# Performance work log

Measured on AMD Instinct MI355X. Metric: run time of the kernel, lower is better.

Reference implementation:

```python
import jax, jax.numpy as jnp
import numpy as np

N_NODES = 100_000
N_EDGES = 1_600_000
NUM_GRAPHS = 512
D1, D2, D3, D5, NUM_CLASSES = 3, 50, 15, 10, 6
BN_EPS = 1e-5


def setup_inputs() -> dict:
    key = jax.random.key(0)
    ks = jax.random.split(key, 16)

    def w(k, shape):
        fan_in = shape[0]
        return jax.random.normal(k, shape, jnp.float32) / np.sqrt(fan_in).astype(np.float32)

    return {
        "x": jax.random.normal(ks[0], (N_NODES, D1), jnp.float32),
        "edge_attr": jax.random.normal(ks[1], (N_EDGES, D1), jnp.float32),
        # edge MLP: Lin(9,50) -> ReLU -> Lin(50,15)
        "edge_w1": w(ks[2], (3 * D1, D2)), "edge_b1": jnp.zeros((D2,), jnp.float32),
        "edge_w2": w(ks[3], (D2, D3)), "edge_b2": jnp.zeros((D3,), jnp.float32),
        # node MLP: Lin(18,50) -> ReLU -> Lin(50,15)
        "node_w1": w(ks[4], (D1 + D3, D2)), "node_b1": jnp.zeros((D2,), jnp.float32),
        "node_w2": w(ks[5], (D2, D3)), "node_b2": jnp.zeros((D3,), jnp.float32),
        # readout head
        "fc1_w": w(ks[6], (D3, D5)), "fc1_b": jnp.zeros((D5,), jnp.float32),
        "bn_gamma": jnp.ones((D5,), jnp.float32), "bn_beta": jnp.zeros((D5,), jnp.float32),
        "fc2_w": w(ks[7], (D5, NUM_CLASSES)), "fc2_b": jnp.zeros((NUM_CLASSES,), jnp.float32),
        # graph structure
        "edge_index": jax.random.randint(ks[8], (2, N_EDGES), 0, N_NODES, jnp.int32),
        "batch": jnp.sort(jax.random.randint(ks[9], (N_NODES,), 0, NUM_GRAPHS, jnp.int32)),
    }


def _segment_mean(vals, idx, num_segments):
    s = jax.ops.segment_sum(vals, idx, num_segments=num_segments)
    c = jax.ops.segment_sum(jnp.ones((vals.shape[0], 1), vals.dtype), idx,
                            num_segments=num_segments)
    return s / jnp.maximum(c, 1.0)


def reference(x, edge_attr,
              edge_w1, edge_b1, edge_w2, edge_b2,
              node_w1, node_b1, node_w2, node_b2,
              fc1_w, fc1_b, bn_gamma, bn_beta, fc2_w, fc2_b,
              edge_index, batch):
    row, col = edge_index[0], edge_index[1]
    # edge model: cat([x[row], x[col], edge_attr]) -> MLP  -> [E, D3]
    e_in = jnp.concatenate([x[row], x[col], edge_attr], axis=1)
    edge_attr2 = jax.nn.relu(e_in @ edge_w1 + edge_b1) @ edge_w2 + edge_b2
    # node model: cat([x[col], edge_attr2]) -> MLP -> scatter_mean over row
    n_in = jnp.concatenate([x[col], edge_attr2], axis=1)  # [E, D1+D3]
    msg = jax.nn.relu(n_in @ node_w1 + node_b1) @ node_w2 + node_b2  # [E, D3]
    x2 = _segment_mean(msg, row, x.shape[0])  # [N, D3]
    # global mean pool per graph -> [G, D3]
    u = _segment_mean(x2, batch, NUM_GRAPHS)
    # head: fc1 -> BatchNorm1d (batch stats) -> relu -> fc2 -> log_softmax
    h = u @ fc1_w + fc1_b
    mu = h.mean(axis=0)
    var = h.var(axis=0)  # biased, matches BN training normalization
    h = bn_gamma * (h - mu) * jax.lax.rsqrt(var + BN_EPS) + bn_beta
    h = jax.nn.relu(h)
    logits = h @ fc2_w + fc2_b
    return jax.nn.log_softmax(logits, axis=1)
```

## Files before the change

kernel.cpp:

```cpp
#include <hip/hip_runtime.h>
#include <hip/hip_bf16.h>
#include <math.h>

#define N_NODES    100000
#define N_EDGES    1600000
#define NUM_GRAPHS 512
#define D2 50
#define D3 15
#define D5 10
#define NCLS 6
#define BN_EPS 1e-5f

#define W_EW1T 0
#define W_EW2T 2560
#define W_NW1T 3712
#define W_NW2T 6272
#define W_TOTAL 7680

#define EDGE_BLOCKS 1024
#define EDGE_WAVES  (EDGE_BLOCKS * 4)
#define TILES32     (N_EDGES / 32)

#define GPAD 17

typedef __attribute__((ext_vector_type(8))) short short8;
typedef __attribute__((ext_vector_type(4))) float float4_;
union BU { unsigned u[4]; short8 s; };

__device__ __forceinline__ unsigned short f2bf(float f) {
    __hip_bfloat16 h = __float2bfloat16(f);
    union { __hip_bfloat16 h; unsigned short u; } c; c.h = h; return c.u;
}
__device__ __forceinline__ unsigned pkbf(float a, float b) {
    unsigned r;
    asm("v_cvt_pk_bf16_f32 %0, %1, %2" : "=v"(r) : "v"(a), "v"(b));
    return r;
}
__device__ __forceinline__ unsigned bp(int s4, unsigned v) {
    return (unsigned)__builtin_amdgcn_ds_bpermute(s4, (int)v);
}

__global__ __launch_bounds__(256) void prep_kernel(
    const float* __restrict__ ew1, const float* __restrict__ eb1,
    const float* __restrict__ ew2, const float* __restrict__ eb2,
    const float* __restrict__ nw1, const float* __restrict__ nb1,
    const float* __restrict__ nw2, const float* __restrict__ nb2,
    unsigned short* __restrict__ wh,
    const float* __restrict__ x, ushort4* __restrict__ x4b,
    const int* __restrict__ edge_index, int* __restrict__ counts,
    const int* __restrict__ batch, float* __restrict__ gsum)
{
    __shared__ int bh[NUM_GRAPHS];
    int gtid = blockIdx.x * 256 + threadIdx.x;
    int gsz = gridDim.x * 256;

    for (int i = threadIdx.x; i < NUM_GRAPHS; i += 256) bh[i] = 0;
    __syncthreads();

    for (int i = gtid; i < W_TOTAL; i += gsz) {
        float v = 0.0f;
        if (i < W_EW2T) {
            int m = i / 40, k = i % 40;
            if (m < 50) {
                if (k < 3)                 v = ew1[k * 50 + m];
                else if (k == 3)           v = eb1[m];
                else if (k >= 4 && k < 7)  v = ew1[(k - 1) * 50 + m];
                else if (k >= 8 && k < 11) v = ew1[(k - 2) * 50 + m];
            }
        } else if (i < W_NW1T) {
            int j = i - W_EW2T; int m = j / 72, k = j % 72;
            if (m < 15) { if (k < 50) v = ew2[k * 15 + m]; else if (k == 50) v = eb2[m]; }
        } else if (i < W_NW2T) {
            int j = i - W_NW1T; int m = j / 40, k = j % 40;
            if (m < 50) {
                if (k < 15)                  v = nw1[(3 + k) * 50 + m];
                else if (k >= 16 && k < 19)  v = nw1[(k - 16) * 50 + m];
                else if (k == 19)            v = nb1[m];
            }
        } else if (i < 7424) {
            int j = i - W_NW2T; int m = j / 72, k = j % 72;
            if (m < 15) { if (k < 50) v = nw2[k * 15 + m]; else if (k == 50) v = nb2[m]; }
        }
        wh[i] = f2bf(v);
    }

    for (int n = gtid; n < N_NODES; n += gsz) {
        ushort4 v;
        v.x = f2bf(x[n * 3 + 0]); v.y = f2bf(x[n * 3 + 1]);
        v.z = f2bf(x[n * 3 + 2]); v.w = 0;
        x4b[n] = v;
        atomicAdd(&bh[batch[n]], 1);
    }

    for (int e = gtid; e < N_EDGES; e += gsz)
        atomicAdd(&counts[edge_index[e]], 1);

    __syncthreads();
    for (int i = threadIdx.x; i < NUM_GRAPHS; i += 256) {
        int v = bh[i];
        if (v) atomicAdd(&gsum[i * 16 + 15], (float)v);
    }
}

struct EIn { unsigned w0, w1, w2, w3, h0, h1; int g; float invd; };

__device__ __forceinline__ EIn load_in(int ebase, int n, int quad,
    const int* __restrict__ edge_index, const ushort4* __restrict__ x4b,
    const float* __restrict__ edge_attr,
    const int* __restrict__ counts, const int* __restrict__ batch)
{
    EIn r; r.w0 = r.w1 = r.w2 = r.w3 = 0; r.h0 = r.h1 = 0; r.g = 0; r.invd = 0.0f;
    int e = ebase + n;
    if (quad == 0) {
        int row = edge_index[e];
        int col = edge_index[N_EDGES + e];
        ushort4 xr = x4b[row];
        ushort4 xc = x4b[col];
        r.w0 = (unsigned)xr.x | ((unsigned)xr.y << 16);
        r.w1 = (unsigned)xr.z | (0x3F80u << 16);
        r.w2 = (unsigned)xc.x | ((unsigned)xc.y << 16);
        r.w3 = (unsigned)xc.z;
        r.g = batch[row];
        r.invd = 1.0f / (float)counts[row];
    } else if (quad == 1) {
        r.w0 = pkbf(edge_attr[e * 3 + 0], edge_attr[e * 3 + 1]);
        r.w1 = pkbf(edge_attr[e * 3 + 2], 0.0f);
    } else if (quad == 2) {
        int col = edge_index[N_EDGES + e];
        ushort4 xc = x4b[col];
        r.h0 = (unsigned)xc.x | ((unsigned)xc.y << 16);
        r.h1 = (unsigned)xc.z | (0x3F80u << 16);
    }
    return r;
}

__device__ __forceinline__ void perm64(const unsigned U[4][2], int s0, int s1, bool hi,
                                       short8& Bc0, short8& Bc1)
{
    BU b0, b1;
    {
        unsigned a0 = bp(s0, U[0][0]), a1 = bp(s0, U[1][0]);
        unsigned a2 = bp(s0, U[0][1]), a3 = bp(s0, U[1][1]);
        unsigned a4 = bp(s1, U[0][0]), a5 = bp(s1, U[1][0]);
        unsigned a6 = bp(s1, U[0][1]), a7 = bp(s1, U[1][1]);
        b0.u[0] = hi ? a1 : a0;
        b0.u[1] = hi ? a3 : a2;
        b0.u[2] = hi ? a5 : a4;
        b0.u[3] = hi ? a7 : a6;
    }
    {
        unsigned a0 = bp(s0, U[2][0]), a1 = bp(s0, U[3][0]);
        unsigned a2 = bp(s0, U[2][1]), a3 = bp(s0, U[3][1]);
        unsigned a4 = bp(s1, U[2][0]), a5 = bp(s1, U[3][0]);
        unsigned a6 = bp(s1, U[2][1]), a7 = bp(s1, U[3][1]);
        b1.u[0] = hi ? a1 : a0;
        b1.u[1] = hi ? a3 : a2;
        b1.u[2] = hi ? a5 : a4;
        b1.u[3] = hi ? a7 : a6;
    }
    Bc0 = b0.s; Bc1 = b1.s;
}

__device__ __forceinline__ short8 perm16(const unsigned U2[2], int s0, int s1,
                                         int quad, unsigned h0, unsigned h1)
{
    BU d;
    d.u[0] = bp(s0, U2[0]);
    d.u[1] = bp(s0, U2[1]);
    d.u[2] = bp(s1, U2[0]);
    d.u[3] = bp(s1, U2[1]);
    if (quad == 2) { d.u[0] = h0; d.u[1] = h1; d.u[2] = 0; d.u[3] = 0; }
    else if (quad == 3) { d.u[0] = 0; d.u[1] = 0; d.u[2] = 0; d.u[3] = 0; }
    return d.s;
}

__global__ __launch_bounds__(256) void edge_fused_kernel(
    const unsigned short* __restrict__ wh_g,
    const ushort4* __restrict__ x4b, const float* __restrict__ edge_attr,
    const int* __restrict__ edge_index,
    const int* __restrict__ counts, const int* __restrict__ batch,
    float* __restrict__ partial)
{
    __shared__ float acc[NUM_GRAPHS * GPAD];
    int tid = threadIdx.x, wave = tid >> 6, lane = tid & 63;
    int n = lane & 15, quad = lane >> 4;

    for (int i = tid; i < NUM_GRAPHS * GPAD; i += 256) acc[i] = 0.0f;
    __syncthreads();

    short8 A1[4], A3[4];
    #pragma unroll
    for (int t4 = 0; t4 < 4; t4++) {
        A1[t4] = *(const short8*)(wh_g + W_EW1T + (t4 * 16 + n) * 40 + quad * 8);
        A3[t4] = *(const short8*)(wh_g + W_NW1T + (t4 * 16 + n) * 40 + quad * 8);
    }
    short8 A2[2], A4[2];
    #pragma unroll
    for (int kc = 0; kc < 2; kc++) {
        A2[kc] = *(const short8*)(wh_g + W_EW2T + n * 72 + kc * 32 + quad * 8);
        A4[kc] = *(const short8*)(wh_g + W_NW2T + n * 72 + kc * 32 + quad * 8);
    }

    int s0 = ((quad & 1) * 32 + n) * 4;
    int s1 = s0 + 64;
    bool hi = (quad & 2) != 0;

    const float4_ Z0 = {0.f, 0.f, 0.f, 0.f};

    int t = blockIdx.x * 4 + wave;
    EIn cur0 = load_in(t * 32,      n, quad, edge_index, x4b, edge_attr, counts, batch);
    EIn cur1 = load_in(t * 32 + 16, n, quad, edge_index, x4b, edge_attr, counts, batch);

    for (;;) {
        int g0 = __shfl(cur0.g, n);
        float q0 = __shfl(cur0.invd, n);
        int g1 = __shfl(cur1.g, n);
        float q1 = __shfl(cur1.invd, n);

        int tn = t + EDGE_WAVES;
        bool more = (tn < TILES32);
        EIn nx0, nx1;
        nx0.w0 = nx0.w1 = nx0.w2 = nx0.w3 = nx0.h0 = nx0.h1 = 0; nx0.g = 0; nx0.invd = 0.f;
        nx1 = nx0;
        if (more) {
            nx0 = load_in(tn * 32,      n, quad, edge_index, x4b, edge_attr, counts, batch);
            nx1 = load_in(tn * 32 + 16, n, quad, edge_index, x4b, edge_attr, counts, batch);
        }

        BU t0, t1;
        t0.u[0] = cur0.w0; t0.u[1] = cur0.w1; t0.u[2] = cur0.w2; t0.u[3] = cur0.w3;
        t1.u[0] = cur1.w0; t1.u[1] = cur1.w1; t1.u[2] = cur1.w2; t1.u[3] = cur1.w3;
        short8 B1a = t0.s, B1b = t1.s;

        unsigned U1a[4][2], U1b[4][2];
        #pragma unroll
        for (int t4 = 0; t4 < 4; t4++) {
            float4_ za = __builtin_amdgcn_mfma_f32_16x16x32_bf16(A1[t4], B1a, Z0, 0, 0, 0);
            float4_ zb = __builtin_amdgcn_mfma_f32_16x16x32_bf16(A1[t4], B1b, Z0, 0, 0, 0);
            U1a[t4][0] = pkbf(fmaxf(za[0], 0.f), fmaxf(za[1], 0.f));
            U1a[t4][1] = pkbf(fmaxf(za[2], 0.f), fmaxf(za[3], 0.f));
            U1b[t4][0] = pkbf(fmaxf(zb[0], 0.f), fmaxf(zb[1], 0.f));
            U1b[t4][1] = pkbf(fmaxf(zb[2], 0.f), fmaxf(zb[3], 0.f));
        }

        short8 B2a0, B2a1, B2b0, B2b1;
        perm64(U1a, s0, s1, hi, B2a0, B2a1);
        perm64(U1b, s0, s1, hi, B2b0, B2b1);
        if (quad == 2) {
            BU fa, fb; fa.s = B2a1; fb.s = B2b1;
            fa.u[1] = (fa.u[1] & 0xFFFF0000u) | 0x3F80u;
            fb.u[1] = (fb.u[1] & 0xFFFF0000u) | 0x3F80u;
            B2a1 = fa.s; B2b1 = fb.s;
        }

        float4_ a2a = __builtin_amdgcn_mfma_f32_16x16x32_bf16(A2[0], B2a0, Z0, 0, 0, 0);
        float4_ a2b = __builtin_amdgcn_mfma_f32_16x16x32_bf16(A2[0], B2b0, Z0, 0, 0, 0);
        a2a = __builtin_amdgcn_mfma_f32_16x16x32_bf16(A2[1], B2a1, a2a, 0, 0, 0);
        a2b = __builtin_amdgcn_mfma_f32_16x16x32_bf16(A2[1], B2b1, a2b, 0, 0, 0);

        unsigned U2a[2] = { pkbf(a2a[0], a2a[1]), pkbf(a2a[2], a2a[3]) };
        unsigned U2b[2] = { pkbf(a2b[0], a2b[1]), pkbf(a2b[2], a2b[3]) };

        short8 B3a = perm16(U2a, s0, s1, quad, cur0.h0, cur0.h1);
        short8 B3b = perm16(U2b, s0, s1, quad, cur1.h0, cur1.h1);

        unsigned U3a[4][2], U3b[4][2];
        #pragma unroll
        for (int t4 = 0; t4 < 4; t4++) {
            float4_ za = __builtin_amdgcn_mfma_f32_16x16x32_bf16(A3[t4], B3a, Z0, 0, 0, 0);
            float4_ zb = __builtin_amdgcn_mfma_f32_16x16x32_bf16(A3[t4], B3b, Z0, 0, 0, 0);
            U3a[t4][0] = pkbf(fmaxf(za[0], 0.f), fmaxf(za[1], 0.f));
            U3a[t4][1] = pkbf(fmaxf(za[2], 0.f), fmaxf(za[3], 0.f));
            U3b[t4][0] = pkbf(fmaxf(zb[0], 0.f), fmaxf(zb[1], 0.f));
            U3b[t4][1] = pkbf(fmaxf(zb[2], 0.f), fmaxf(zb[3], 0.f));
        }

        short8 B4a0, B4a1, B4b0, B4b1;
        perm64(U3a, s0, s1, hi, B4a0, B4a1);
        perm64(U3b, s0, s1, hi, B4b0, B4b1);
        if (quad == 2) {
            BU fa, fb; fa.s = B4a1; fb.s = B4b1;
            fa.u[1] = (fa.u[1] & 0xFFFF0000u) | 0x3F80u;
            fb.u[1] = (fb.u[1] & 0xFFFF0000u) | 0x3F80u;
            B4a1 = fa.s; B4b1 = fb.s;
        }

        float4_ ma = __builtin_amdgcn_mfma_f32_16x16x32_bf16(A4[0], B4a0, Z0, 0, 0, 0);
        float4_ mb = __builtin_amdgcn_mfma_f32_16x16x32_bf16(A4[0], B4b0, Z0, 0, 0, 0);
        ma = __builtin_amdgcn_mfma_f32_16x16x32_bf16(A4[1], B4a1, ma, 0, 0, 0);
        mb = __builtin_amdgcn_mfma_f32_16x16x32_bf16(A4[1], B4b1, mb, 0, 0, 0);

        float* a0 = &acc[g0 * GPAD + quad * 4];
        float* a1 = &acc[g1 * GPAD + quad * 4];
        atomicAdd(&a0[0], ma[0] * q0);
        atomicAdd(&a0[1], ma[1] * q0);
        atomicAdd(&a0[2], ma[2] * q0);
        atomicAdd(&a1[0], mb[0] * q1);
        atomicAdd(&a1[1], mb[1] * q1);
        atomicAdd(&a1[2], mb[2] * q1);
        if (quad != 3) {
            atomicAdd(&a0[3], ma[3] * q0);
            atomicAdd(&a1[3], mb[3] * q1);
        }

        if (!more) break;
        cur0 = nx0; cur1 = nx1; t = tn;
    }

    __syncthreads();
    float* pb = partial + (size_t)blockIdx.x * (NUM_GRAPHS * 16);
    for (int i = tid; i < NUM_GRAPHS * 16; i += 256)
        pb[i] = acc[(i >> 4) * GPAD + (i & 15)];
}

__global__ __launch_bounds__(256) void reduce_kernel(
    const float* __restrict__ partial, float* __restrict__ gsum)
{
    __shared__ float red[256];
    int g = blockIdx.x;
    float s = 0.0f;
    for (int j = threadIdx.x; j < EDGE_BLOCKS * 16; j += 256) {
        int b = j >> 4, c = j & 15;
        s += partial[(size_t)b * (NUM_GRAPHS * 16) + g * 16 + c];
    }
    red[threadIdx.x] = s;
    __syncthreads();
    if (threadIdx.x < 16) {
        float t = 0.0f;
        #pragma unroll
        for (int k = 0; k < 16; k++) t += red[k * 16 + threadIdx.x];
        gsum[g * 16 + threadIdx.x] += t;
    }
}

__global__ __launch_bounds__(512) void head_kernel(
    const float* __restrict__ gsum,
    const float* __restrict__ fc1w, const float* __restrict__ fc1b,
    const float* __restrict__ gamma, const float* __restrict__ beta,
    const float* __restrict__ fc2w, const float* __restrict__ fc2b,
    float* __restrict__ out)
{
    __shared__ float ssum[D5], ssq[D5], smu[D5], sistd[D5];
    int g = threadIdx.x;
    if (g < D5) { ssum[g] = 0.0f; ssq[g] = 0.0f; }
    __syncthreads();

    const float* src = gsum + (size_t)g * 16;
    float inv = 1.0f / fmaxf(src[15], 1.0f);
    float u[D3];
    #pragma unroll
    for (int k = 0; k < D3; k++) u[k] = src[k] * inv;

    float h[D5];
    #pragma unroll
    for (int c = 0; c < D5; c++) h[c] = fc1b[c];
    #pragma unroll
    for (int k = 0; k < D3; k++) {
        float v = u[k];
        #pragma unroll
        for (int c = 0; c < D5; c++) h[c] = fmaf(v, fc1w[k * D5 + c], h[c]);
    }

    int lane = threadIdx.x & 63;
    #pragma unroll
    for (int c = 0; c < D5; c++) {
        float v = h[c];
        float v2 = v * v;
        #pragma unroll
        for (int off = 32; off >= 1; off >>= 1) {
            v  += __shfl_xor(v,  off);
            v2 += __shfl_xor(v2, off);
        }
        if (lane == 0) { atomicAdd(&ssum[c], v); atomicAdd(&ssq[c], v2); }
    }
    __syncthreads();
    if (g < D5) {
        float mu = ssum[g] * (1.0f / NUM_GRAPHS);
        float var = ssq[g] * (1.0f / NUM_GRAPHS) - mu * mu;
        smu[g] = mu;
        sistd[g] = rsqrtf(var + BN_EPS);
    }
    __syncthreads();

    float hn[D5];
    #pragma unroll
    for (int c = 0; c < D5; c++) {
        float v = gamma[c] * (h[c] - smu[c]) * sistd[c] + beta[c];
        hn[c] = fmaxf(v, 0.0f);
    }

    float lg[NCLS];
    #pragma unroll
    for (int j = 0; j < NCLS; j++) lg[j] = fc2b[j];
    #pragma unroll
    for (int c = 0; c < D5; c++) {
        float v = hn[c];
        #pragma unroll
        for (int j = 0; j < NCLS; j++) lg[j] = fmaf(v, fc2w[c * NCLS + j], lg[j]);
    }

    float m = lg[0];
    #pragma unroll
    for (int j = 1; j < NCLS; j++) m = fmaxf(m, lg[j]);
    float se = 0.0f;
    #pragma unroll
    for (int j = 0; j < NCLS; j++) se += expf(lg[j] - m);
    float lse = logf(se);
    #pragma unroll
    for (int j = 0; j < NCLS; j++) out[g * NCLS + j] = lg[j] - m - lse;
}

extern "C" void kernel_launch(void* const* d_in, const int* in_sizes, int n_in,
                              void* d_out, int out_size, void* d_ws, size_t ws_size,
                              hipStream_t stream) {
    const float* x         = (const float*)d_in[0];
    const float* edge_attr = (const float*)d_in[1];
    const float* ew1  = (const float*)d_in[2];
    const float* eb1  = (const float*)d_in[3];
    const float* ew2  = (const float*)d_in[4];
    const float* eb2  = (const float*)d_in[5];
    const float* nw1  = (const float*)d_in[6];
    const float* nb1  = (const float*)d_in[7];
    const float* nw2  = (const float*)d_in[8];
    const float* nb2  = (const float*)d_in[9];
    const float* fc1w = (const float*)d_in[10];
    const float* fc1b = (const float*)d_in[11];
    const float* gamma= (const float*)d_in[12];
    const float* beta = (const float*)d_in[13];
    const float* fc2w = (const float*)d_in[14];
    const float* fc2b = (const float*)d_in[15];
    const int* edge_index = (const int*)d_in[16];
    const int* batch      = (const int*)d_in[17];

    char* p = (char*)d_ws;
    float* partial = (float*)p;        p += (size_t)EDGE_BLOCKS * NUM_GRAPHS * 16 * sizeof(float);
    int* counts  = (int*)p;            p += (size_t)N_NODES * sizeof(int);
    ushort4* x4b = (ushort4*)p;        p += (size_t)N_NODES * sizeof(ushort4);
    float* gsum  = (float*)p;          p += (size_t)NUM_GRAPHS * 16 * sizeof(float);
    unsigned short* wh = (unsigned short*)p; p += W_TOTAL * sizeof(unsigned short);

    hipMemsetAsync(counts, 0, (size_t)N_NODES * sizeof(int), stream);
    hipMemsetAsync(gsum, 0, (size_t)NUM_GRAPHS * 16 * sizeof(float), stream);

    int egrid = (N_EDGES + 255) / 256;

    prep_kernel<<<egrid, 256, 0, stream>>>(
        ew1, eb1, ew2, eb2, nw1, nb1, nw2, nb2, wh,
        x, x4b, edge_index, counts, batch, gsum);
    edge_fused_kernel<<<EDGE_BLOCKS, 256, 0, stream>>>(
        wh, x4b, edge_attr, edge_index, counts, batch, partial);
    reduce_kernel<<<NUM_GRAPHS, 256, 0, stream>>>(partial, gsum);
    head_kernel<<<1, 512, 0, stream>>>(
        gsum, fc1w, fc1b, gamma, beta, fc2w, fc2b, (float*)d_out);
}
```

Before: 382.2 us.

## Precompute packed per-edge graph id and degree, use exact edge iteration count

Adds a pre-pass kernel that packs batch[row] and counts[row] into one 32-bit word per edge. The edge kernel then does one coalesced load instead of two dependent gathers, and swaps the divide for a hardware reciprocal. The edge grid becomes 1250 blocks so every wave gets the same number of tiles, which gives a fixed-count loop with no branch. The LDS accumulator padding also shrinks from 17 to 15. The cost is an extra kernel launch plus 6.4 MB written and read back, and the packing assumes degree below 2^23.

```diff
diff --git a/kernel.cpp b/kernel.cpp
--- a/kernel.cpp
+++ b/kernel.cpp
@@ -17,11 +17,12 @@
 #define W_NW2T 6272
 #define W_TOTAL 7680
 
-#define EDGE_BLOCKS 1024
+#define TILES32     (N_EDGES / 32)
+#define EDGE_BLOCKS 1250
 #define EDGE_WAVES  (EDGE_BLOCKS * 4)
-#define TILES32     (N_EDGES / 32)
-
-#define GPAD 17
+#define EDGE_ITERS  (TILES32 / EDGE_WAVES)
+
+#define GPAD 15
 
 typedef __attribute__((ext_vector_type(8))) short short8;
 typedef __attribute__((ext_vector_type(4))) float float4_;
@@ -102,14 +103,24 @@
     }
 }
 
-struct EIn { unsigned w0, w1, w2, w3, h0, h1; int g; float invd; };
+__global__ __launch_bounds__(256) void gd_kernel(
+    const int* __restrict__ edge_index, const int* __restrict__ counts,
+    const int* __restrict__ batch, unsigned* __restrict__ gd)
+{
+    int e = blockIdx.x * 256 + threadIdx.x;
+    if (e < N_EDGES) {
+        int row = edge_index[e];
+        gd[e] = ((unsigned)batch[row] << 23) | (unsigned)counts[row];
+    }
+}
+
+struct EIn { unsigned w0, w1, w2, w3, h0, h1, gdp; };
 
 __device__ __forceinline__ EIn load_in(int ebase, int n, int quad,
     const int* __restrict__ edge_index, const ushort4* __restrict__ x4b,
-    const float* __restrict__ edge_attr,
-    const int* __restrict__ counts, const int* __restrict__ batch)
-{
-    EIn r; r.w0 = r.w1 = r.w2 = r.w3 = 0; r.h0 = r.h1 = 0; r.g = 0; r.invd = 0.0f;
+    const float* __restrict__ edge_attr, const unsigned* __restrict__ gdb)
+{
+    EIn r; r.w0 = r.w1 = r.w2 = r.w3 = 0; r.h0 = r.h1 = 0; r.gdp = 0;
     int e = ebase + n;
     if (quad == 0) {
         int row = edge_index[e];
@@ -120,8 +131,7 @@
         r.w1 = (unsigned)xr.z | (0x3F80u << 16);
         r.w2 = (unsigned)xc.x | ((unsigned)xc.y << 16);
         r.w3 = (unsigned)xc.z;
-        r.g = batch[row];
-        r.invd = 1.0f / (float)counts[row];
+        r.gdp = gdb[e];
     } else if (quad == 1) {
         r.w0 = pkbf(edge_attr[e * 3 + 0], edge_attr[e * 3 + 1]);
         r.w1 = pkbf(edge_attr[e * 3 + 2], 0.0f);
@@ -177,8 +187,7 @@
 __global__ __launch_bounds__(256) void edge_fused_kernel(
     const unsigned short* __restrict__ wh_g,
     const ushort4* __restrict__ x4b, const float* __restrict__ edge_attr,
-    const int* __restrict__ edge_index,
-    const int* __restrict__ counts, const int* __restrict__ batch,
+    const int* __restrict__ edge_index, const unsigned* __restrict__ gdb,
     float* __restrict__ partial)
 {
     __shared__ float acc[NUM_GRAPHS * GPAD];
@@ -207,29 +216,16 @@
 
     const float4_ Z0 = {0.f, 0.f, 0.f, 0.f};
 
-    int t = blockIdx.x * 4 + wave;
-    EIn cur0 = load_in(t * 32,      n, quad, edge_index, x4b, edge_attr, counts, batch);
-    EIn cur1 = load_in(t * 32 + 16, n, quad, edge_index, x4b, edge_attr, counts, batch);
-
-    for (;;) {
-        int g0 = __shfl(cur0.g, n);
-        float q0 = __shfl(cur0.invd, n);
-        int g1 = __shfl(cur1.g, n);
-        float q1 = __shfl(cur1.invd, n);
-
-        int tn = t + EDGE_WAVES;
-        bool more = (tn < TILES32);
-        EIn nx0, nx1;
-        nx0.w0 = nx0.w1 = nx0.w2 = nx0.w3 = nx0.h0 = nx0.h1 = 0; nx0.g = 0; nx0.invd = 0.f;
-        nx1 = nx0;
-        if (more) {
-            nx0 = load_in(tn * 32,      n, quad, edge_index, x4b, edge_attr, counts, batch);
-            nx1 = load_in(tn * 32 + 16, n, quad, edge_index, x4b, edge_attr, counts, batch);
-        }
+    auto body = [&](const EIn& c0, const EIn& c1) {
+        unsigned gp0 = (unsigned)__shfl((int)c0.gdp, n);
+        unsigned gp1 = (unsigned)__shfl((int)c1.gdp, n);
+        int g0 = (int)(gp0 >> 23), g1 = (int)(gp1 >> 23);
+        float q0 = __builtin_amdgcn_rcpf((float)(gp0 & 0x7FFFFFu));
+        float q1 = __builtin_amdgcn_rcpf((float)(gp1 & 0x7FFFFFu));
 
         BU t0, t1;
-        t0.u[0] = cur0.w0; t0.u[1] = cur0.w1; t0.u[2] = cur0.w2; t0.u[3] = cur0.w3;
-        t1.u[0] = cur1.w0; t1.u[1] = cur1.w1; t1.u[2] = cur1.w2; t1.u[3] = cur1.w3;
+        t0.u[0] = c0.w0; t0.u[1] = c0.w1; t0.u[2] = c0.w2; t0.u[3] = c0.w3;
+        t1.u[0] = c1.w0; t1.u[1] = c1.w1; t1.u[2] = c1.w2; t1.u[3] = c1.w3;
         short8 B1a = t0.s, B1b = t1.s;
 
         unsigned U1a[4][2], U1b[4][2];
@@ -261,8 +257,8 @@
         unsigned U2a[2] = { pkbf(a2a[0], a2a[1]), pkbf(a2a[2], a2a[3]) };
         unsigned U2b[2] = { pkbf(a2b[0], a2b[1]), pkbf(a2b[2], a2b[3]) };
 
-        short8 B3a = perm16(U2a, s0, s1, quad, cur0.h0, cur0.h1);
-        short8 B3b = perm16(U2b, s0, s1, quad, cur1.h0, cur1.h1);
+        short8 B3a = perm16(U2a, s0, s1, quad, c0.h0, c0.h1);
+        short8 B3b = perm16(U2b, s0, s1, quad, c1.h0, c1.h1);
 
         unsigned U3a[4][2], U3b[4][2];
         #pragma unroll
@@ -302,15 +298,27 @@
             atomicAdd(&a0[3], ma[3] * q0);
             atomicAdd(&a1[3], mb[3] * q1);
         }
-
-        if (!more) break;
+    };
+
+    int t = blockIdx.x * 4 + wave;
+    EIn cur0 = load_in(t * 32,      n, quad, edge_index, x4b, edge_attr, gdb);
+    EIn cur1 = load_in(t * 32 + 16, n, quad, edge_index, x4b, edge_attr, gdb);
+
+    for (int it = 0; it < EDGE_ITERS - 1; it++) {
+        int tn = t + EDGE_WAVES;
+        EIn nx0 = load_in(tn * 32,      n, quad, edge_index, x4b, edge_attr, gdb);
+        EIn nx1 = load_in(tn * 32 + 16, n, quad, edge_index, x4b, edge_attr, gdb);
+        body(cur0, cur1);
         cur0 = nx0; cur1 = nx1; t = tn;
     }
+    body(cur0, cur1);
 
     __syncthreads();
     float* pb = partial + (size_t)blockIdx.x * (NUM_GRAPHS * 16);
-    for (int i = tid; i < NUM_GRAPHS * 16; i += 256)
-        pb[i] = acc[(i >> 4) * GPAD + (i & 15)];
+    for (int i = tid; i < NUM_GRAPHS * 16; i += 256) {
+        int c = i & 15;
+        pb[i] = (c < 15) ? acc[(i >> 4) * GPAD + c] : 0.0f;
+    }
 }
 
 __global__ __launch_bounds__(256) void reduce_kernel(
@@ -435,6 +443,7 @@
     char* p = (char*)d_ws;
     float* partial = (float*)p;        p += (size_t)EDGE_BLOCKS * NUM_GRAPHS * 16 * sizeof(float);
     int* counts  = (int*)p;            p += (size_t)N_NODES * sizeof(int);
+    unsigned* gd = (unsigned*)p;       p += (size_t)N_EDGES * sizeof(unsigned);
     ushort4* x4b = (ushort4*)p;        p += (size_t)N_NODES * sizeof(ushort4);
     float* gsum  = (float*)p;          p += (size_t)NUM_GRAPHS * 16 * sizeof(float);
     unsigned short* wh = (unsigned short*)p; p += W_TOTAL * sizeof(unsigned short);
@@ -447,8 +456,9 @@
     prep_kernel<<<egrid, 256, 0, stream>>>(
         ew1, eb1, ew2, eb2, nw1, nb1, nw2, nb2, wh,
         x, x4b, edge_index, counts, batch, gsum);
+    gd_kernel<<<egrid, 256, 0, stream>>>(edge_index, counts, batch, gd);
     edge_fused_kernel<<<EDGE_BLOCKS, 256, 0, stream>>>(
-        wh, x4b, edge_attr, edge_index, counts, batch, partial);
+        wh, x4b, edge_attr, edge_index, gd, partial);
     reduce_kernel<<<NUM_GRAPHS, 256, 0, stream>>>(partial, gsum);
     head_kernel<<<1, 512, 0, stream>>>(
         gsum, fc1w, fc1b, gamma, beta, fc2w, fc2b, (float*)d_out);
```

After: 401.1 us. +4.9%, slower.
